# Optimization experiments

Measured on AMD Instinct MI355X. Metric: run time of the kernel, lower is better.

Reference implementation:

```python
import jax, jax.numpy as jnp
import numpy as np

GATE_INIT_BIAS = -0.6931471805599453  # -log(2)

def mish(x):
    return x * jnp.tanh(jax.nn.softplus(x))

def setup_inputs() -> dict:
    key = jax.random.key(0)
    ks = jax.random.split(key, 24)
    B = 262144
    x = jax.random.normal(ks[0], (B, 18), dtype=jnp.float32)
    band = jax.random.randint(ks[1], (B,), 0, 9).astype(jnp.float32)
    x = x.at[:, 17].set(band)
    def lin(k, fan_in, shape):
        bound = 1.0 / np.sqrt(fan_in)
        return jax.random.uniform(k, shape, jnp.float32, -bound, bound)
    inp = {
        'x': x,
        # trunk: 15->512->256 (Mish)
        'tw1': lin(ks[2], 15, (15, 512)),  'tb1': lin(ks[3], 15, (512,)),
        'tw2': lin(ks[4], 512, (512, 256)), 'tb2': lin(ks[5], 512, (256,)),
        # 9 band heads: 256->128->1, stacked on leading axis
        'hw1': lin(ks[6], 256, (9, 256, 128)), 'hb1': lin(ks[7], 256, (9, 128)),
        'hw2': lin(ks[8], 128, (9, 128)),      'hb2': lin(ks[9], 128, (9,)),
        # sun scaler head 256->64->1 (final layer zero weight, bias = gate_init_bias)
        'sw1': lin(ks[10], 256, (256, 64)), 'sb1': lin(ks[11], 256, (64,)),
        'sw2': jnp.zeros((64, 1), jnp.float32), 'sb2': jnp.full((1,), GATE_INIT_BIAS, jnp.float32),
        # storm scaler head
        'stw1': lin(ks[12], 256, (256, 64)), 'stb1': lin(ks[13], 256, (64,)),
        'stw2': jnp.zeros((64, 1), jnp.float32), 'stb2': jnp.full((1,), GATE_INIT_BIAS, jnp.float32),
        # monotonic sidecars: 1->8->1, softplus-positivized weights
        'sun_w1': lin(ks[14], 1, (1, 8)),  'sun_b1': lin(ks[15], 1, (8,)),
        'sun_w2': lin(ks[16], 8, (8, 1)),  'sun_b2': lin(ks[17], 8, (1,)),
        'storm_w1': lin(ks[18], 1, (1, 8)), 'storm_b1': lin(ks[19], 1, (8,)),
        'storm_w2': lin(ks[20], 8, (8, 1)), 'storm_b2': lin(ks[21], 8, (1,)),
    }
    return inp

def monotonic_mlp(v, w1, b1, w2, b2):
    # MonotonicMLP: positivity via softplus on weights, tanh hidden activation
    h = jnp.tanh(v @ jax.nn.softplus(w1) + b1)
    return h @ jax.nn.softplus(w2) + b2  # [B,1]

def reference(x, tw1, tb1, tw2, tb2, hw1, hb1, hw2, hb2,
              sw1, sb1, sw2, sb2, stw1, stb1, stw2, stb2,
              sun_w1, sun_b1, sun_w2, sun_b2,
              storm_w1, storm_b1, storm_w2, storm_b2):
    x_deep = x[:, :15]
    x_sfi = x[:, 15:16]
    x_kp = x[:, 16:17]
    band = x[:, 17].astype(jnp.int32)  # [B]

    # trunk
    t = mish(mish(x_deep @ tw1 + tb1) @ tw2 + tb2)  # [B,256]

    # all 9 band heads densely (faithful to original), then gather
    hh = mish(jnp.einsum('bd,kdh->bkh', t, hw1) + hb1)       # [B,9,128]
    all_heads = jnp.einsum('bkh,kh->bk', hh, hw2) + hb2      # [B,9]
    base_snr = jnp.take_along_axis(all_heads, band[:, None], axis=1)  # [B,1]

    sun_logit = mish(t @ sw1 + sb1) @ sw2 + sb2      # [B,1]
    storm_logit = mish(t @ stw1 + stb1) @ stw2 + stb2
    sun_gate = jax.nn.sigmoid(sun_logit)
    storm_gate = jax.nn.sigmoid(storm_logit)

    return base_snr + sun_gate * monotonic_mlp(x_sfi, sun_w1, sun_b1, sun_w2, sun_b2) \
                    + storm_gate * monotonic_mlp(x_kp, storm_w1, storm_b1, storm_w2, storm_b2)
```

## Files before the change

### kernel.cpp

```cpp
#include <hip/hip_runtime.h>
#include <cstdint>

typedef unsigned short u16;
typedef __attribute__((ext_vector_type(8))) __bf16 bf16x8;
typedef __attribute__((ext_vector_type(4))) float f32x4;

#define MFMA16(a, b, c) __builtin_amdgcn_mfma_f32_16x16x32_bf16((a), (b), (c), 0, 0, 0)

__device__ __forceinline__ u16 f2b(float f) {
    union { float f; unsigned u; } v; v.f = f;
    unsigned r = v.u + 0x7fffu + ((v.u >> 16) & 1u);
    return (u16)(r >> 16);
}
__device__ __forceinline__ float b2f(u16 h) {
    union { unsigned u; float f; } v; v.u = ((unsigned)h) << 16; return v.f;
}
__device__ __forceinline__ float fast_rcp(float x) { return __builtin_amdgcn_rcpf(x); }
__device__ __forceinline__ float mish_f(float x) {
    float e = __expf(fminf(x, 40.0f));
    float u = 1.0f + e;
    float u2 = u * u;
    return x * (u2 - 1.0f) * fast_rcp(u2 + 1.0f);
}
__device__ __forceinline__ float tanh_f(float y) {
    float e = __expf(2.0f * y);
    return 1.0f - 2.0f * fast_rcp(e + 1.0f);
}
__device__ __forceinline__ float sigmoid_f(float y) {
    return fast_rcp(1.0f + __expf(-y));
}
__device__ __forceinline__ float splus(float w) { return log1pf(__expf(w)); }

#define WS_PERM      0u
#define WS_GSC       1048576u
#define WS_GOFF      1048640u
#define WS_BBAND     1048704u
#define WS_BSTART    1065152u
#define WS_BNROWS    1081600u
#define WS_SP        1098048u
#define WS_GPART     1098176u
#define WS_W1P       1116608u
#define WS_W2F       1149376u
#define WS_HW1F      1411520u
#define WS_SWF       2001344u
#define WS_STWF      2034112u
#define WS_NEEDED    2066880u

#define PACK_BLOCKS  512


__global__ void k_pack(const float* __restrict__ x, int B,
                       const float* __restrict__ tw1, const float* __restrict__ tw2,
                       const float* __restrict__ hw1,
                       const float* __restrict__ sw1, const float* __restrict__ stw1,
                       const float* __restrict__ sun_w1, const float* __restrict__ sun_w2,
                       const float* __restrict__ storm_w1, const float* __restrict__ storm_w2,
                       u16* __restrict__ W1p, u16* __restrict__ W2f, u16* __restrict__ HWf,
                       u16* __restrict__ SWf, u16* __restrict__ STWf,
                       float* __restrict__ sp, int* __restrict__ gpart)
{
    __shared__ int h[9];
    int ltid = threadIdx.x;
    int tid = blockIdx.x * blockDim.x + ltid;
    if (ltid < 9) h[ltid] = 0;
    __syncthreads();
    for (int i = tid; i < B; i += PACK_BLOCKS * 256) {
        int b = (int)x[i * 18 + 17];
        atomicAdd(&h[b], 1);
    }

    if (tid < 32) {
        const float* srcs[4] = { sun_w1, sun_w2, storm_w1, storm_w2 };
        float w = srcs[tid >> 3][tid & 7];
        sp[tid] = splus(w);
    }
    const int total = 16384 + 131072 + 294912 + 16384 + 16384;
    for (int i = tid; i < total; i += PACK_BLOCKS * 256) {
        int idx = i;
        if (idx < 16384) {
            int n = idx >> 5, k = idx & 31;
            W1p[idx] = (k < 15) ? f2b(tw1[k * 512 + n]) : (u16)0;
        } else if ((idx -= 16384) < 131072) {
            int tile = idx >> 9, within = idx & 511;
            int lane = within >> 3, j = within & 7;
            int nt = tile >> 4, kb = tile & 15;
            int n = nt * 16 + (lane & 15);
            int k = kb * 32 + (lane >> 4) * 8 + j;
            W2f[idx] = f2b(tw2[k * 256 + n]);
        } else if ((idx -= 131072) < 294912) {
            int g = idx >> 15, r = idx & 32767;
            int tile = r >> 9, within = r & 511;
            int lane = within >> 3, j = within & 7;
            int nt = tile >> 3, kb = tile & 7;
            int n = nt * 16 + (lane & 15);
            int k = kb * 32 + (lane >> 4) * 8 + j;
            HWf[idx] = f2b(hw1[(g * 256 + k) * 128 + n]);
        } else if ((idx -= 294912) < 16384) {
            int tile = idx >> 9, within = idx & 511;
            int lane = within >> 3, j = within & 7;
            int nt = tile >> 3, kb = tile & 7;
            int n = nt * 16 + (lane & 15);
            int k = kb * 32 + (lane >> 4) * 8 + j;
            SWf[idx] = f2b(sw1[k * 64 + n]);
        } else {
            idx -= 16384;
            int tile = idx >> 9, within = idx & 511;
            int lane = within >> 3, j = within & 7;
            int nt = tile >> 3, kb = tile & 7;
            int n = nt * 16 + (lane & 15);
            int k = kb * 32 + (lane >> 4) * 8 + j;
            STWf[idx] = f2b(stw1[k * 64 + n]);
        }
    }
    __syncthreads();
    if (ltid < 9) gpart[blockIdx.x * 9 + ltid] = h[ltid];
}

__global__ void k_table(const int* __restrict__ gpart, int* __restrict__ goff,
                        int* __restrict__ gsc, int* __restrict__ blk_band,
                        int* __restrict__ blk_start, int* __restrict__ blk_nrows, int nblk_max)
{
    __shared__ int s_goff[10], s_bstart[10], s_cnt[9];
    int tid = threadIdx.x;
    if (tid < 9) {
        int s = 0;
        for (int b = 0; b < PACK_BLOCKS; ++b) s += gpart[b * 9 + tid];
        s_cnt[tid] = s;
    }
    __syncthreads();
    if (tid == 0) {
        int off = 0, boff = 0;
        for (int g = 0; g < 9; ++g) {
            s_goff[g] = off; goff[g] = off;
            s_bstart[g] = boff;
            off += s_cnt[g];
            boff += (s_cnt[g] + 63) >> 6;
        }
        s_goff[9] = off; goff[9] = off;
        s_bstart[9] = boff;
        for (int g = 0; g < 9; ++g) gsc[g] = 0;
    }
    __syncthreads();
    for (int b = tid; b < nblk_max; b += blockDim.x) {
        int band = -1, loc = 0;
        for (int g = 0; g < 9; ++g)
            if (b >= s_bstart[g] && b < s_bstart[g + 1]) { band = g; loc = b - s_bstart[g]; }
        blk_band[b] = band;
        if (band >= 0) {
            blk_start[b] = s_goff[band] + loc * 64;
            int rem = s_cnt[band] - loc * 64;
            blk_nrows[b] = rem < 64 ? rem : 64;
        } else { blk_start[b] = 0; blk_nrows[b] = 0; }
    }
}

__global__ void k_scatter(const float* __restrict__ x, const int* __restrict__ goff,
                          int* __restrict__ gsc, int* __restrict__ perm, int B)
{
    __shared__ int wcnt[4][9];
    __shared__ int wpre[4][9];
    __shared__ int gbase[9];
    int tid = threadIdx.x;
    int lane = tid & 63, wave = tid >> 6;
    int i = blockIdx.x * blockDim.x + tid;
    int band = -1, rank = 0;
    if (i < B) band = (int)x[i * 18 + 17];
    for (int k = 0; k < 9; ++k) {
        unsigned long long m = __ballot(band == k);
        if (band == k) rank = __popcll(m & ((1ull << lane) - 1ull));
        if (lane == 0) wcnt[wave][k] = __popcll(m);
    }
    __syncthreads();
    if (tid < 9) {
        int k = tid, run = 0;
        for (int w = 0; w < 4; ++w) { wpre[w][k] = run; run += wcnt[w][k]; }
        gbase[k] = (run > 0) ? atomicAdd(&gsc[k], run) : 0;
    }
    __syncthreads();
    if (i < B && band >= 0) {
        int pos = goff[band] + gbase[band] + wpre[wave][band] + rank;
        perm[pos] = i;
    }
}

__global__ __launch_bounds__(512, 4) void k_main(
                       const float* __restrict__ x,
                       const int* __restrict__ perm,
                       const int* __restrict__ blk_band,
                       const int* __restrict__ blk_start,
                       const int* __restrict__ blk_nrows,
                       const u16* __restrict__ W1p, const u16* __restrict__ W2f,
                       const u16* __restrict__ HWf,
                       const u16* __restrict__ SWf, const u16* __restrict__ STWf,
                       const float* __restrict__ tb1, const float* __restrict__ tb2,
                       const float* __restrict__ hb1, const float* __restrict__ hw2,
                       const float* __restrict__ hb2,
                       const float* __restrict__ sb1, const float* __restrict__ sw2,
                       const float* __restrict__ sb2,
                       const float* __restrict__ stb1, const float* __restrict__ stw2,
                       const float* __restrict__ stb2,
                       const float* __restrict__ sp,
                       const float* __restrict__ sun_b1, const float* __restrict__ sun_b2,
                       const float* __restrict__ storm_b1, const float* __restrict__ storm_b2,
                       float* __restrict__ out)
{
    int bb = blk_band[blockIdx.x];
    if (bb < 0) return;
    int rstart = blk_start[blockIdx.x];
    int nrows  = blk_nrows[blockIdx.x];

    __shared__ u16 xA[64][32];
    __shared__ int rowsL[64];
    __shared__ float sfiL[64], kpL[64];
    __shared__ u16 buf[2][64][136];
    __shared__ float headp[8][64], sunp[4][64], stormp[4][64];

    int tid = threadIdx.x;
    int lane = tid & 63, wave = tid >> 6;
    int quad = lane >> 4, l15 = lane & 15;

    if (tid < 64) {
        int r = rstart + (tid < nrows ? tid : 0);
        rowsL[tid] = perm[r];
    }
    for (int i = tid; i < 64 * 32; i += 512) ((u16*)xA)[i] = 0;
    __syncthreads();
    for (int i = tid; i < 64 * 18; i += 512) {
        int r = i / 18, c = i - r * 18;
        float v = x[rowsL[r] * 18 + c];
        if (c < 15) xA[r][c] = f2b(v);
        else if (c == 15) sfiL[r] = v;
        else if (c == 16) kpL[r] = v;
    }
    __syncthreads();

    bf16x8 ax[4];
#pragma unroll
    for (int mt = 0; mt < 4; ++mt)
        ax[mt] = *(const bf16x8*)&xA[mt * 16 + l15][quad * 8];

    f32x4 acc2[2][4] = {};

    for (int c = 0; c < 4; ++c) {
        f32x4 acc1[4] = {};
        {
            int ncol = c * 128 + wave * 16 + l15;
            bf16x8 bw = *(const bf16x8*)&W1p[ncol * 32 + quad * 8];
#pragma unroll
            for (int mt = 0; mt < 4; ++mt)
                acc1[mt] = MFMA16(ax[mt], bw, acc1[mt]);
        }
        u16 (*bufc)[136] = buf[c & 1];
        {
            int ccol = wave * 16 + l15;
            float bias = tb1[c * 128 + ccol];
#pragma unroll
            for (int mt = 0; mt < 4; ++mt)
#pragma unroll
                for (int r = 0; r < 4; ++r)
                    bufc[mt * 16 + quad * 4 + r][ccol] = f2b(mish_f(acc1[mt][r] + bias));
        }
        __syncthreads();
        for (int ks = 0; ks < 4; ++ks) {
            bf16x8 a2[4];
#pragma unroll
            for (int mt = 0; mt < 4; ++mt)
                a2[mt] = *(const bf16x8*)&bufc[mt * 16 + l15][ks * 32 + quad * 8];
            int kb = c * 4 + ks;
#pragma unroll
            for (int ntl = 0; ntl < 2; ++ntl) {
                int nt = wave * 2 + ntl;
                bf16x8 bw = *(const bf16x8*)&W2f[((nt * 16 + kb) << 9) + lane * 8];
#pragma unroll
                for (int mt = 0; mt < 4; ++mt)
                    acc2[ntl][mt] = MFMA16(a2[mt], bw, acc2[ntl][mt]);
            }
        }
    }
    __syncthreads();

    u16 (*tmat)[264] = (u16(*)[264])buf;
#pragma unroll
    for (int ntl = 0; ntl < 2; ++ntl) {
        int col = wave * 32 + ntl * 16 + l15;
        float bias = tb2[col];
#pragma unroll
        for (int mt = 0; mt < 4; ++mt)
#pragma unroll
            for (int r = 0; r < 4; ++r)
                tmat[mt * 16 + quad * 4 + r][col] = f2b(mish_f(acc2[ntl][mt][r] + bias));
    }
    __syncthreads();

    f32x4 acch[4] = {}, accg[4] = {};
    const u16* Hw = HWf + bb * 32768;
    const u16* Gw = (wave < 4) ? SWf : STWf;
    int gnt = wave & 3;
    for (int kb = 0; kb < 8; ++kb) {
        bf16x8 a3[4];
#pragma unroll
        for (int mt = 0; mt < 4; ++mt)
            a3[mt] = *(const bf16x8*)&tmat[mt * 16 + l15][kb * 32 + quad * 8];
        bf16x8 bh = *(const bf16x8*)&Hw[((wave * 8 + kb) << 9) + lane * 8];
        bf16x8 bg = *(const bf16x8*)&Gw[((gnt * 8 + kb) << 9) + lane * 8];
#pragma unroll
        for (int mt = 0; mt < 4; ++mt) {
            acch[mt] = MFMA16(a3[mt], bh, acch[mt]);
            accg[mt] = MFMA16(a3[mt], bg, accg[mt]);
        }
    }

    float hsum[4][4];
    {
        int col = wave * 16 + l15;
        float hb = hb1[bb * 128 + col];
        float wv = hw2[bb * 128 + col];
#pragma unroll
        for (int mt = 0; mt < 4; ++mt)
#pragma unroll
            for (int r = 0; r < 4; ++r)
                hsum[mt][r] = mish_f(acch[mt][r] + hb) * wv;
    }
    float gsum[4][4];
    {
        int n = gnt * 16 + l15;
        float gb = (wave < 4) ? sb1[n] : stb1[n];
        float gw = (wave < 4) ? sw2[n] : stw2[n];
#pragma unroll
        for (int mt = 0; mt < 4; ++mt)
#pragma unroll
            for (int r = 0; r < 4; ++r)
                gsum[mt][r] = mish_f(accg[mt][r] + gb) * gw;
    }
#pragma unroll
    for (int off = 1; off < 16; off <<= 1)
#pragma unroll
        for (int mt = 0; mt < 4; ++mt)
#pragma unroll
            for (int r = 0; r < 4; ++r) {
                hsum[mt][r] += __shfl_xor(hsum[mt][r], off, 64);
                gsum[mt][r] += __shfl_xor(gsum[mt][r], off, 64);
            }
    if (l15 == 0)
#pragma unroll
        for (int mt = 0; mt < 4; ++mt)
#pragma unroll
            for (int r = 0; r < 4; ++r) {
                int row = mt * 16 + quad * 4 + r;
                headp[wave][row] = hsum[mt][r];
                if (wave < 4) sunp[wave][row] = gsum[mt][r];
                else          stormp[wave - 4][row] = gsum[mt][r];
            }
    __syncthreads();

    if (tid < 64 && tid < nrows) {
        int row = tid;
        float head = hb2[bb];
#pragma unroll
        for (int w = 0; w < 8; ++w) head += headp[w][row];
        float sl = sb2[0], tl = stb2[0];
#pragma unroll
        for (int w = 0; w < 4; ++w) { sl += sunp[w][row]; tl += stormp[w][row]; }
        float sg = sigmoid_f(sl);
        float tg = sigmoid_f(tl);
        float v1 = sfiL[row], v2 = kpL[row];
        float sun_val = sun_b2[0], storm_val = storm_b2[0];
#pragma unroll
        for (int j = 0; j < 8; ++j) {
            sun_val   += tanh_f(v1 * sp[j]      + sun_b1[j])   * sp[8 + j];
            storm_val += tanh_f(v2 * sp[16 + j] + storm_b1[j]) * sp[24 + j];
        }
        out[rowsL[row]] = head + sg * sun_val + tg * storm_val;
    }
}

__global__ __launch_bounds__(64) void k_simple(
    const float* __restrict__ x,
    const float* __restrict__ tw1, const float* __restrict__ tb1,
    const float* __restrict__ tw2, const float* __restrict__ tb2,
    const float* __restrict__ hw1, const float* __restrict__ hb1,
    const float* __restrict__ hw2, const float* __restrict__ hb2,
    const float* __restrict__ sw1, const float* __restrict__ sb1,
    const float* __restrict__ sw2, const float* __restrict__ sb2,
    const float* __restrict__ stw1, const float* __restrict__ stb1,
    const float* __restrict__ stw2, const float* __restrict__ stb2,
    const float* __restrict__ sun_w1, const float* __restrict__ sun_b1,
    const float* __restrict__ sun_w2, const float* __restrict__ sun_b2,
    const float* __restrict__ storm_w1, const float* __restrict__ storm_b1,
    const float* __restrict__ storm_w2, const float* __restrict__ storm_b2,
    float* __restrict__ out)
{
    __shared__ u16 t_lds[256 * 64];

    const int lane = threadIdx.x;
    const int r = blockIdx.x * 64 + lane;

    float xr[15];
#pragma unroll
    for (int k = 0; k < 15; ++k) xr[k] = x[r * 18 + k];
    const float sfi = x[r * 18 + 15];
    const float kp  = x[r * 18 + 16];
    const int band  = (int)x[r * 18 + 17];

    for (int tc = 0; tc < 4; ++tc) {
        float acc[64];
#pragma unroll
        for (int j = 0; j < 64; ++j) acc[j] = 0.0f;
        for (int n = 0; n < 512; ++n) {
            float p = tb1[n];
#pragma unroll
            for (int k = 0; k < 15; ++k) p += xr[k] * tw1[k * 512 + n];
            const float a1n = mish_f(p);
            const float* w2 = &tw2[n * 256 + tc * 64];
#pragma unroll
            for (int j = 0; j < 64; ++j) acc[j] += a1n * w2[j];
        }
#pragma unroll
        for (int j = 0; j < 64; ++j)
            t_lds[(tc * 64 + j) * 64 + lane] = f2b(mish_f(acc[j] + tb2[tc * 64 + j]));
    }
    __syncthreads();

    float head_val = 0.0f;
    for (int g = 0; g < 9; ++g) {
        float hs = 0.0f;
        for (int hc = 0; hc < 2; ++hc) {
            float pre[64];
#pragma unroll
            for (int j = 0; j < 64; ++j) pre[j] = 0.0f;
            for (int d = 0; d < 256; ++d) {
                const float td = b2f(t_lds[d * 64 + lane]);
                const float* wv = &hw1[g * 32768 + d * 128 + hc * 64];
#pragma unroll
                for (int j = 0; j < 64; ++j) pre[j] += td * wv[j];
            }
#pragma unroll
            for (int j = 0; j < 64; ++j) {
                const int h = hc * 64 + j;
                hs += mish_f(pre[j] + hb1[g * 128 + h]) * hw2[g * 128 + h];
            }
        }
        head_val += (band == g) ? (hs + hb2[g]) : 0.0f;
    }

    float pre_s[64], pre_t[64];
#pragma unroll
    for (int j = 0; j < 64; ++j) { pre_s[j] = 0.0f; pre_t[j] = 0.0f; }
    for (int d = 0; d < 256; ++d) {
        const float td = b2f(t_lds[d * 64 + lane]);
        const float* ws1 = &sw1[d * 64];
        const float* wt1 = &stw1[d * 64];
#pragma unroll
        for (int j = 0; j < 64; ++j) {
            pre_s[j] += td * ws1[j];
            pre_t[j] += td * wt1[j];
        }
    }
    float ls = sb2[0], lt = stb2[0];
#pragma unroll
    for (int j = 0; j < 64; ++j) {
        ls += mish_f(pre_s[j] + sb1[j]) * sw2[j];
        lt += mish_f(pre_t[j] + stb1[j]) * stw2[j];
    }
    const float sg = sigmoid_f(ls);
    const float tg = sigmoid_f(lt);

    float sun_val = sun_b2[0], storm_val = storm_b2[0];
#pragma unroll
    for (int j = 0; j < 8; ++j) {
        sun_val   += tanh_f(sfi * splus(sun_w1[j])  + sun_b1[j])   * splus(sun_w2[j]);
        storm_val += tanh_f(kp * splus(storm_w1[j]) + storm_b1[j]) * splus(storm_w2[j]);
    }

    out[r] = head_val + sg * sun_val + tg * storm_val;
}

extern "C" void kernel_launch(void* const* d_in, const int* in_sizes, int n_in,
                              void* d_out, int out_size, void* d_ws, size_t ws_size,
                              hipStream_t stream) {
    (void)n_in; (void)out_size;
    const float* x        = (const float*)d_in[0];
    const float* tw1      = (const float*)d_in[1];
    const float* tb1      = (const float*)d_in[2];
    const float* tw2      = (const float*)d_in[3];
    const float* tb2      = (const float*)d_in[4];
    const float* hw1      = (const float*)d_in[5];
    const float* hb1      = (const float*)d_in[6];
    const float* hw2      = (const float*)d_in[7];
    const float* hb2      = (const float*)d_in[8];
    const float* sw1      = (const float*)d_in[9];
    const float* sb1      = (const float*)d_in[10];
    const float* sw2      = (const float*)d_in[11];
    const float* sb2      = (const float*)d_in[12];
    const float* stw1     = (const float*)d_in[13];
    const float* stb1     = (const float*)d_in[14];
    const float* stw2     = (const float*)d_in[15];
    const float* stb2     = (const float*)d_in[16];
    const float* sun_w1   = (const float*)d_in[17];
    const float* sun_b1   = (const float*)d_in[18];
    const float* sun_w2   = (const float*)d_in[19];
    const float* sun_b2   = (const float*)d_in[20];
    const float* storm_w1 = (const float*)d_in[21];
    const float* storm_b1 = (const float*)d_in[22];
    const float* storm_w2 = (const float*)d_in[23];
    const float* storm_b2 = (const float*)d_in[24];

    const int B = in_sizes[0] / 18;

    if (ws_size < (size_t)WS_NEEDED) {
        k_simple<<<B / 64, 64, 0, stream>>>(x, tw1, tb1, tw2, tb2, hw1, hb1, hw2, hb2,
                                            sw1, sb1, sw2, sb2, stw1, stb1, stw2, stb2,
                                            sun_w1, sun_b1, sun_w2, sun_b2,
                                            storm_w1, storm_b1, storm_w2, storm_b2,
                                            (float*)d_out);
        return;
    }

    char* ws = (char*)d_ws;
    int*   perm      = (int*)(ws + WS_PERM);
    int*   gsc       = (int*)(ws + WS_GSC);
    int*   goff      = (int*)(ws + WS_GOFF);
    int*   blk_band  = (int*)(ws + WS_BBAND);
    int*   blk_start = (int*)(ws + WS_BSTART);
    int*   blk_nrows = (int*)(ws + WS_BNROWS);
    float* sp        = (float*)(ws + WS_SP);
    int*   gpart     = (int*)(ws + WS_GPART);
    u16*   W1p       = (u16*)(ws + WS_W1P);
    u16*   W2f       = (u16*)(ws + WS_W2F);
    u16*   HWf       = (u16*)(ws + WS_HW1F);
    u16*   SWf       = (u16*)(ws + WS_SWF);
    u16*   STWf      = (u16*)(ws + WS_STWF);

    int nblk = B / 64 + 16;

    k_pack<<<PACK_BLOCKS, 256, 0, stream>>>(x, B, tw1, tw2, hw1, sw1, stw1,
                                            sun_w1, sun_w2, storm_w1, storm_w2,
                                            W1p, W2f, HWf, SWf, STWf, sp, gpart);
    k_table<<<1, 256, 0, stream>>>(gpart, goff, gsc, blk_band, blk_start, blk_nrows, nblk);
    k_scatter<<<(B + 255) / 256, 256, 0, stream>>>(x, goff, gsc, perm, B);
    k_main<<<nblk, 512, 0, stream>>>(x, perm, blk_band, blk_start, blk_nrows,
                                     W1p, W2f, HWf, SWf, STWf,
                                     tb1, tb2, hb1, hw2, hb2,
                                     sb1, sw2, sb2, stb1, stw2, stb2,
                                     sp, sun_b1, sun_b2, storm_b1, storm_b2,
                                     (float*)d_out);
}
```

Measured before the change: 334.0 us.

## Cache band bytes for scatter, share LDS via union, raise occupancy hint

The pack kernel now writes each row's band as a byte array, so the scatter kernel reads compact bytes instead of strided floats from x. In k_main, the reduction scratch now shares LDS with the xA tile through a union, which lowers shared memory per block. The launch bounds minimum-blocks hint goes from 4 to 8, which pushes the compiler toward fewer registers and higher occupancy. Software float-to-bf16 rounding is replaced with the hardware conversion; this risks register spills under the tighter register budget.

Result: slower. 411.4 us (+23.2%).

```diff
diff --git a/kernel.cpp b/kernel.cpp
--- a/kernel.cpp
+++ b/kernel.cpp
@@ -2,6 +2,7 @@
 #include <cstdint>
 
 typedef unsigned short u16;
+typedef unsigned char u8;
 typedef __attribute__((ext_vector_type(8))) __bf16 bf16x8;
 typedef __attribute__((ext_vector_type(4))) float f32x4;
 
@@ -11,6 +12,9 @@
     union { float f; unsigned u; } v; v.f = f;
     unsigned r = v.u + 0x7fffu + ((v.u >> 16) & 1u);
     return (u16)(r >> 16);
+}
+__device__ __forceinline__ u16 f2b_hw(float f) {
+    union { __bf16 h; u16 u; } cv; cv.h = (__bf16)f; return cv.u;
 }
 __device__ __forceinline__ float b2f(u16 h) {
     union { unsigned u; float f; } v; v.u = ((unsigned)h) << 16; return v.f;
@@ -39,12 +43,13 @@
 #define WS_BNROWS    1081600u
 #define WS_SP        1098048u
 #define WS_GPART     1098176u
-#define WS_W1P       1116608u
-#define WS_W2F       1149376u
-#define WS_HW1F      1411520u
-#define WS_SWF       2001344u
-#define WS_STWF      2034112u
-#define WS_NEEDED    2066880u
+#define WS_BANDS     1116608u
+#define WS_W1P       1378752u
+#define WS_W2F       1411520u
+#define WS_HW1F      1673664u
+#define WS_SWF       2263488u
+#define WS_STWF      2296256u
+#define WS_NEEDED    2329024u
 
 #define PACK_BLOCKS  512
 
@@ -57,7 +62,8 @@
                        const float* __restrict__ storm_w1, const float* __restrict__ storm_w2,
                        u16* __restrict__ W1p, u16* __restrict__ W2f, u16* __restrict__ HWf,
                        u16* __restrict__ SWf, u16* __restrict__ STWf,
-                       float* __restrict__ sp, int* __restrict__ gpart)
+                       float* __restrict__ sp, int* __restrict__ gpart,
+                       u8* __restrict__ bands)
 {
     __shared__ int h[9];
     int ltid = threadIdx.x;
@@ -66,6 +72,7 @@
     __syncthreads();
     for (int i = tid; i < B; i += PACK_BLOCKS * 256) {
         int b = (int)x[i * 18 + 17];
+        bands[i] = (u8)b;
         atomicAdd(&h[b], 1);
     }
 
@@ -154,7 +161,7 @@
     }
 }
 
-__global__ void k_scatter(const float* __restrict__ x, const int* __restrict__ goff,
+__global__ void k_scatter(const u8* __restrict__ bands, const int* __restrict__ goff,
                           int* __restrict__ gsc, int* __restrict__ perm, int B)
 {
     __shared__ int wcnt[4][9];
@@ -164,7 +171,7 @@
     int lane = tid & 63, wave = tid >> 6;
     int i = blockIdx.x * blockDim.x + tid;
     int band = -1, rank = 0;
-    if (i < B) band = (int)x[i * 18 + 17];
+    if (i < B) band = (int)bands[i];
     for (int k = 0; k < 9; ++k) {
         unsigned long long m = __ballot(band == k);
         if (band == k) rank = __popcll(m & ((1ull << lane) - 1ull));
@@ -183,7 +190,7 @@
     }
 }
 
-__global__ __launch_bounds__(512, 4) void k_main(
+__global__ __launch_bounds__(512, 8) void k_main(
                        const float* __restrict__ x,
                        const int* __restrict__ perm,
                        const int* __restrict__ blk_band,
@@ -209,11 +216,13 @@
     int rstart = blk_start[blockIdx.x];
     int nrows  = blk_nrows[blockIdx.x];
 
-    __shared__ u16 xA[64][32];
+    __shared__ union {
+        u16 xA[64][32];
+        float red[16][64];
+    } su;
     __shared__ int rowsL[64];
     __shared__ float sfiL[64], kpL[64];
     __shared__ u16 buf[2][64][136];
-    __shared__ float headp[8][64], sunp[4][64], stormp[4][64];
 
     int tid = threadIdx.x;
     int lane = tid & 63, wave = tid >> 6;
@@ -223,12 +232,12 @@
         int r = rstart + (tid < nrows ? tid : 0);
         rowsL[tid] = perm[r];
     }
-    for (int i = tid; i < 64 * 32; i += 512) ((u16*)xA)[i] = 0;
+    for (int i = tid; i < 64 * 32; i += 512) ((u16*)su.xA)[i] = 0;
     __syncthreads();
     for (int i = tid; i < 64 * 18; i += 512) {
         int r = i / 18, c = i - r * 18;
         float v = x[rowsL[r] * 18 + c];
-        if (c < 15) xA[r][c] = f2b(v);
+        if (c < 15) su.xA[r][c] = f2b_hw(v);
         else if (c == 15) sfiL[r] = v;
         else if (c == 16) kpL[r] = v;
     }
@@ -237,7 +246,7 @@
     bf16x8 ax[4];
 #pragma unroll
     for (int mt = 0; mt < 4; ++mt)
-        ax[mt] = *(const bf16x8*)&xA[mt * 16 + l15][quad * 8];
+        ax[mt] = *(const bf16x8*)&su.xA[mt * 16 + l15][quad * 8];
 
     f32x4 acc2[2][4] = {};
 
@@ -258,7 +267,7 @@
             for (int mt = 0; mt < 4; ++mt)
 #pragma unroll
                 for (int r = 0; r < 4; ++r)
-                    bufc[mt * 16 + quad * 4 + r][ccol] = f2b(mish_f(acc1[mt][r] + bias));
+                    bufc[mt * 16 + quad * 4 + r][ccol] = f2b_hw(mish_f(acc1[mt][r] + bias));
         }
         __syncthreads();
         for (int ks = 0; ks < 4; ++ks) {
@@ -288,7 +297,7 @@
         for (int mt = 0; mt < 4; ++mt)
 #pragma unroll
             for (int r = 0; r < 4; ++r)
-                tmat[mt * 16 + quad * 4 + r][col] = f2b(mish_f(acc2[ntl][mt][r] + bias));
+                tmat[mt * 16 + quad * 4 + r][col] = f2b_hw(mish_f(acc2[ntl][mt][r] + bias));
     }
     __syncthreads();
 
@@ -347,9 +356,8 @@
 #pragma unroll
             for (int r = 0; r < 4; ++r) {
                 int row = mt * 16 + quad * 4 + r;
-                headp[wave][row] = hsum[mt][r];
-                if (wave < 4) sunp[wave][row] = gsum[mt][r];
-                else          stormp[wave - 4][row] = gsum[mt][r];
+                su.red[wave][row] = hsum[mt][r];
+                su.red[8 + wave][row] = gsum[mt][r];
             }
     __syncthreads();
 
@@ -357,10 +365,10 @@
         int row = tid;
         float head = hb2[bb];
 #pragma unroll
-        for (int w = 0; w < 8; ++w) head += headp[w][row];
+        for (int w = 0; w < 8; ++w) head += su.red[w][row];
         float sl = sb2[0], tl = stb2[0];
 #pragma unroll
-        for (int w = 0; w < 4; ++w) { sl += sunp[w][row]; tl += stormp[w][row]; }
+        for (int w = 0; w < 4; ++w) { sl += su.red[8 + w][row]; tl += su.red[12 + w][row]; }
         float sg = sigmoid_f(sl);
         float tg = sigmoid_f(tl);
         float v1 = sfiL[row], v2 = kpL[row];
@@ -525,6 +533,7 @@
     int*   blk_nrows = (int*)(ws + WS_BNROWS);
     float* sp        = (float*)(ws + WS_SP);
     int*   gpart     = (int*)(ws + WS_GPART);
+    u8*    bands     = (u8*)(ws + WS_BANDS);
     u16*   W1p       = (u16*)(ws + WS_W1P);
     u16*   W2f       = (u16*)(ws + WS_W2F);
     u16*   HWf       = (u16*)(ws + WS_HW1F);
@@ -535,9 +544,9 @@
 
     k_pack<<<PACK_BLOCKS, 256, 0, stream>>>(x, B, tw1, tw2, hw1, sw1, stw1,
                                             sun_w1, sun_w2, storm_w1, storm_w2,
-                                            W1p, W2f, HWf, SWf, STWf, sp, gpart);
+                                            W1p, W2f, HWf, SWf, STWf, sp, gpart, bands);
     k_table<<<1, 256, 0, stream>>>(gpart, goff, gsc, blk_band, blk_start, blk_nrows, nblk);
-    k_scatter<<<(B + 255) / 256, 256, 0, stream>>>(x, goff, gsc, perm, B);
+    k_scatter<<<(B + 255) / 256, 256, 0, stream>>>(bands, goff, gsc, perm, B);
     k_main<<<nblk, 512, 0, stream>>>(x, perm, blk_band, blk_start, blk_nrows,
                                      W1p, W2f, HWf, SWf, STWf,
                                      tb1, tb2, hb1, hw2, hb2,
```
